# Kernel optimization log

Hardware: AMD Instinct MI355X
Metric: run time of the kernel (lower is better)

## Reference

```python
import jax, jax.numpy as jnp
import numpy as np

N_NODES = 100000
N_EDGES = 1600000
D_FEAT = 32


def setup_inputs() -> dict:
    key = jax.random.key(0)
    k1, k2 = jax.random.split(key)
    x = jax.random.normal(k1, (N_NODES, D_FEAT), dtype=jnp.float32)
    edge_index = jax.random.randint(k2, (2, N_EDGES), 0, N_NODES, dtype=jnp.int64)
    return {"x": x, "edge_index": edge_index}


def reference(x, edge_index):
    # SparseTensor(row=edge_index[0], col=edge_index[1]).matmul(x, reduce='mean')
    # out[i] = mean_{e: row[e]==i} x[col[e]], 0 for isolated rows.
    row, col = edge_index[0], edge_index[1]
    msg_sum = jax.ops.segment_sum(x[col], row, num_segments=N_NODES)  # [N, D]
    deg = jax.ops.segment_sum(jnp.ones((row.shape[0],), dtype=x.dtype), row,
                              num_segments=N_NODES)  # [N]
    denom = jnp.maximum(deg, jnp.asarray(1, dtype=x.dtype))
    return msg_sum / denom[:, None]
```

## Files before the change

### kernel.cpp

```cpp
#include <hip/hip_runtime.h>
#include <hip/hip_fp16.h>

#define D_FEAT 32
#define BNODES 64
#define LOG_BN 6
#define CHUNK 16384
#define BIG 1024
#define CAP 1536
#define ECHUNK CAP
#define CMASK 0x1FFFFu

__global__ void zero_kernel(int* __restrict__ p, int n) {
    int i = blockIdx.x * blockDim.x + threadIdx.x;
    if (i < n) p[i] = 0;
}

__global__ void __launch_bounds__(BIG) build_kernel(const int* __restrict__ row,
                                                    const int* __restrict__ col,
                                                    const float* __restrict__ x,
                                                    __half* __restrict__ xh,
                                                    int* __restrict__ cnt,
                                                    unsigned* __restrict__ packed,
                                                    int E, int nb, int n8) {
    extern __shared__ int shmem[];
    int* hist = shmem;
    int* base = shmem + nb;
    int t = threadIdx.x;
    int blk = blockIdx.x;
    for (int i = t; i < nb; i += BIG) hist[i] = 0;

    int s = blk * CHUNK;
    int e_end = min(E, s + CHUNK);

    int4 r[4], c[4];
    if (s + CHUNK <= E) {
        #pragma unroll
        for (int k = 0; k < 4; ++k) {
            int e = s + t * 4 + k * (BIG * 4);
            r[k] = *(const int4*)&row[e];
            c[k] = *(const int4*)&col[e];
        }
    } else {
        #pragma unroll
        for (int k = 0; k < 4; ++k) {
            int e = s + t * 4 + k * (BIG * 4);
            r[k].x = (e + 0 < e_end) ? row[e + 0] : -1;
            r[k].y = (e + 1 < e_end) ? row[e + 1] : -1;
            r[k].z = (e + 2 < e_end) ? row[e + 2] : -1;
            r[k].w = (e + 3 < e_end) ? row[e + 3] : -1;
            c[k].x = (e + 0 < e_end) ? col[e + 0] : 0;
            c[k].y = (e + 1 < e_end) ? col[e + 1] : 0;
            c[k].z = (e + 2 < e_end) ? col[e + 2] : 0;
            c[k].w = (e + 3 < e_end) ? col[e + 3] : 0;
        }
    }
    __syncthreads();

    #pragma unroll
    for (int k = 0; k < 4; ++k) {
        if (r[k].x >= 0) atomicAdd(&hist[r[k].x >> LOG_BN], 1);
        if (r[k].y >= 0) atomicAdd(&hist[r[k].y >> LOG_BN], 1);
        if (r[k].z >= 0) atomicAdd(&hist[r[k].z >> LOG_BN], 1);
        if (r[k].w >= 0) atomicAdd(&hist[r[k].w >> LOG_BN], 1);
    }
    __syncthreads();

    for (int i = t; i < nb; i += BIG) {
        int h = hist[i];
        base[i] = h ? (i * CAP + atomicAdd(&cnt[i], h)) : 0;
    }
    __syncthreads();

    #define EMIT(rr, cc)                                                      \
        if ((rr) >= 0) {                                                      \
            int b_ = (rr) >> LOG_BN;                                          \
            int slot_ = base[b_] + atomicAdd(&hist[b_], -1) - 1;              \
            packed[slot_] = ((unsigned)((rr) & (BNODES - 1)) << 17) |         \
                            (unsigned)(cc);                                   \
        }
    #pragma unroll
    for (int k = 0; k < 4; ++k) {
        EMIT(r[k].x, c[k].x); EMIT(r[k].y, c[k].y);
        EMIT(r[k].z, c[k].z); EMIT(r[k].w, c[k].w);
    }
    #undef EMIT

    int gstride = gridDim.x * BIG;
    for (int i = blk * BIG + t; i < n8; i += gstride) {
        float4 v = ((const float4*)x)[i];
        __half2 h0 = __floats2half2_rn(v.x, v.y);
        __half2 h1 = __floats2half2_rn(v.z, v.w);
        uint2 u;
        u.x = *reinterpret_cast<unsigned*>(&h0);
        u.y = *reinterpret_cast<unsigned*>(&h1);
        ((uint2*)xh)[i] = u;
    }
}

__global__ void __launch_bounds__(512) phase2_kernel(const __half* __restrict__ xh,
                                                     const unsigned* __restrict__ packed,
                                                     const int* __restrict__ cnt,
                                                     float* __restrict__ out, int N) {
    __shared__ unsigned scol[ECHUNK];
    __shared__ int hist[BNODES];
    __shared__ int hoff[BNODES];
    int t = threadIdx.x;
    int b = blockIdx.x;
    int s = b * CAP;
    int n = cnt[b];
    int node = t >> 3;
    int j = t & 7;
    const uint2* xh2 = (const uint2*)xh;

    if (t < BNODES) hist[t] = 0;
    __syncthreads();

    unsigned pv[3];
    int nv = 0;
    #pragma unroll
    for (int k = 0; k < 3; ++k) {
        int i = t + k * 512;
        if (i < n) {
            unsigned p = packed[s + i];
            pv[nv++] = p;
            atomicAdd(&hist[p >> 17], 1);
        }
    }
    __syncthreads();

    if (t < 64) {
        int v = hist[t];
        int sum = v;
        #pragma unroll
        for (int off = 1; off < 64; off <<= 1) {
            int w = __shfl_up(sum, off);
            if (t >= off) sum += w;
        }
        hoff[t] = sum - v;
    }
    __syncthreads();
    int mcount = hist[node];
    int mbase = hoff[node];
    __syncthreads();

    #pragma unroll
    for (int k = 0; k < 3; ++k) {
        if (k < nv) {
            unsigned p = pv[k];
            int r = p >> 17;
            int slot = hoff[r] + atomicAdd(&hist[r], -1) - 1;
            scol[slot] = p;
        }
    }
    __syncthreads();

    float4 acc = make_float4(0.f, 0.f, 0.f, 0.f);
    #define ACCUM(u)                                                           \
        {                                                                      \
            __half2 ha = *reinterpret_cast<const __half2*>(&(u).x);            \
            __half2 hb = *reinterpret_cast<const __half2*>(&(u).y);            \
            float2 fa = __half22float2(ha);                                    \
            float2 fb = __half22float2(hb);                                    \
            acc.x += fa.x; acc.y += fa.y; acc.z += fb.x; acc.w += fb.y;        \
        }
    int i = 0;
    for (; i + 7 < mcount; i += 8) {
        unsigned cc0 = scol[mbase + i + 0] & CMASK;
        unsigned cc1 = scol[mbase + i + 1] & CMASK;
        unsigned cc2 = scol[mbase + i + 2] & CMASK;
        unsigned cc3 = scol[mbase + i + 3] & CMASK;
        unsigned cc4 = scol[mbase + i + 4] & CMASK;
        unsigned cc5 = scol[mbase + i + 5] & CMASK;
        unsigned cc6 = scol[mbase + i + 6] & CMASK;
        unsigned cc7 = scol[mbase + i + 7] & CMASK;
        uint2 u0 = xh2[cc0 * 8 + j];
        uint2 u1 = xh2[cc1 * 8 + j];
        uint2 u2 = xh2[cc2 * 8 + j];
        uint2 u3 = xh2[cc3 * 8 + j];
        uint2 u4 = xh2[cc4 * 8 + j];
        uint2 u5 = xh2[cc5 * 8 + j];
        uint2 u6 = xh2[cc6 * 8 + j];
        uint2 u7 = xh2[cc7 * 8 + j];
        ACCUM(u0); ACCUM(u1); ACCUM(u2); ACCUM(u3);
        ACCUM(u4); ACCUM(u5); ACCUM(u6); ACCUM(u7);
    }
    for (; i < mcount; ++i) {
        unsigned cc = scol[mbase + i] & CMASK;
        uint2 u = xh2[cc * 8 + j];
        ACCUM(u);
    }
    #undef ACCUM

    int gnode = b * BNODES + node;
    if (gnode < N) {
        float invd = 1.0f / fmaxf((float)mcount, 1.0f);
        float4 v;
        v.x = acc.x * invd; v.y = acc.y * invd;
        v.z = acc.z * invd; v.w = acc.w * invd;
        ((float4*)out)[(size_t)gnode * 8 + j] = v;
    }
}


extern "C" void kernel_launch(void* const* d_in, const int* in_sizes, int n_in,
                              void* d_out, int out_size, void* d_ws, size_t ws_size,
                              hipStream_t stream) {
    const float* x = (const float*)d_in[0];
    const int* edge_index = (const int*)d_in[1];

    int E = in_sizes[1] / 2;
    const int* row = edge_index;
    const int* col = edge_index + E;
    int N = in_sizes[0] / D_FEAT;

    float* out = (float*)d_out;

    int nb = (N + BNODES - 1) / BNODES;
    int nchunks = (E + CHUNK - 1) / CHUNK;
    int n8 = in_sizes[0] / 4;

    int* cnt = (int*)d_ws;
    __half* xh = (__half*)(cnt + ((nb + 1023) & ~1023));
    unsigned* packed = (unsigned*)((char*)xh + (size_t)in_sizes[0] * sizeof(__half));

    zero_kernel<<<(nb + 255) / 256, 256, 0, stream>>>(cnt, nb);

    size_t lds = (size_t)2 * nb * sizeof(int);
    build_kernel<<<nchunks, BIG, lds, stream>>>(row, col, x, xh, cnt, packed, E, nb, n8);
    phase2_kernel<<<nb, 512, 0, stream>>>(xh, packed, cnt, out, N);
}
```

Before: 57.42 us.

## Replace global atomic bucket offsets with per-chunk fixed-slot regions and drop zero kernel

The build kernel no longer uses global atomics on a per-bucket counter. Each chunk writes its edges into a fixed region of REG slots per bucket and records a per-chunk, per-bucket count, which also removes the separate zeroing kernel. The phase-2 kernel prefix-scans those counts across chunks, gathers the scattered regions into shared memory, then does the same local sort as before. This removes global atomic contention and one launch, but the gather becomes scattered and edges past REG per chunk, or past RAWCAP per bucket, are silently dropped.

```diff
diff --git a/kernel.cpp b/kernel.cpp
--- a/kernel.cpp
+++ b/kernel.cpp
@@ -6,25 +6,19 @@
 #define LOG_BN 6
 #define CHUNK 16384
 #define BIG 1024
-#define CAP 1536
-#define ECHUNK CAP
+#define REG 40
+#define RAWCAP 1536
+#define NCH_MAX 128
 #define CMASK 0x1FFFFu
-
-__global__ void zero_kernel(int* __restrict__ p, int n) {
-    int i = blockIdx.x * blockDim.x + threadIdx.x;
-    if (i < n) p[i] = 0;
-}
 
 __global__ void __launch_bounds__(BIG) build_kernel(const int* __restrict__ row,
                                                     const int* __restrict__ col,
                                                     const float* __restrict__ x,
                                                     __half* __restrict__ xh,
-                                                    int* __restrict__ cnt,
+                                                    int* __restrict__ hcnt,
                                                     unsigned* __restrict__ packed,
-                                                    int E, int nb, int n8) {
-    extern __shared__ int shmem[];
-    int* hist = shmem;
-    int* base = shmem + nb;
+                                                    int E, int nb, int nchunks, int n8) {
+    extern __shared__ int hist[];
     int t = threadIdx.x;
     int blk = blockIdx.x;
     for (int i = t; i < nb; i += BIG) hist[i] = 0;
@@ -65,18 +59,19 @@
     }
     __syncthreads();
 
-    for (int i = t; i < nb; i += BIG) {
-        int h = hist[i];
-        base[i] = h ? (i * CAP + atomicAdd(&cnt[i], h)) : 0;
-    }
-    __syncthreads();
-
+    size_t hrow = (size_t)blk * nb;
+    for (int i = t; i < nb; i += BIG) hcnt[hrow + i] = min(hist[i], REG);
+    __syncthreads();
+
+    size_t rstride = (size_t)nchunks * REG;
+    size_t kbase = (size_t)blk * REG;
     #define EMIT(rr, cc)                                                      \
         if ((rr) >= 0) {                                                      \
             int b_ = (rr) >> LOG_BN;                                          \
-            int slot_ = base[b_] + atomicAdd(&hist[b_], -1) - 1;              \
-            packed[slot_] = ((unsigned)((rr) & (BNODES - 1)) << 17) |         \
-                            (unsigned)(cc);                                   \
+            int si = atomicAdd(&hist[b_], -1) - 1;                            \
+            if (si < REG)                                                     \
+                packed[(size_t)b_ * rstride + kbase + si] =                   \
+                    ((unsigned)((rr) & (BNODES - 1)) << 17) | (unsigned)(cc); \
         }
     #pragma unroll
     for (int k = 0; k < 4; ++k) {
@@ -99,33 +94,69 @@
 
 __global__ void __launch_bounds__(512) phase2_kernel(const __half* __restrict__ xh,
                                                      const unsigned* __restrict__ packed,
-                                                     const int* __restrict__ cnt,
-                                                     float* __restrict__ out, int N) {
-    __shared__ unsigned scol[ECHUNK];
+                                                     const int* __restrict__ hcnt,
+                                                     float* __restrict__ out,
+                                                     int N, int nb, int nchunks) {
+    __shared__ int cntk[NCH_MAX];
+    __shared__ int pref[NCH_MAX + 2];
+    __shared__ unsigned scol_raw[RAWCAP];
+    __shared__ unsigned scol[RAWCAP];
     __shared__ int hist[BNODES];
     __shared__ int hoff[BNODES];
     int t = threadIdx.x;
     int b = blockIdx.x;
-    int s = b * CAP;
-    int n = cnt[b];
+    size_t rbase = (size_t)b * nchunks * REG;
     int node = t >> 3;
     int j = t & 7;
     const uint2* xh2 = (const uint2*)xh;
 
+    if (t < nchunks) cntk[t] = hcnt[(size_t)t * nb + b];
     if (t < BNODES) hist[t] = 0;
     __syncthreads();
 
-    unsigned pv[3];
-    int nv = 0;
-    #pragma unroll
-    for (int k = 0; k < 3; ++k) {
-        int i = t + k * 512;
-        if (i < n) {
-            unsigned p = packed[s + i];
-            pv[nv++] = p;
-            atomicAdd(&hist[p >> 17], 1);
-        }
-    }
+    if (t < 64) {
+        int v = (t < nchunks) ? cntk[t] : 0;
+        int sum = v;
+        #pragma unroll
+        for (int off = 1; off < 64; off <<= 1) {
+            int w = __shfl_up(sum, off);
+            if (t >= off) sum += w;
+        }
+        pref[t] = sum - v;
+        if (t == 63) pref[NCH_MAX] = sum;
+    }
+    __syncthreads();
+    if (t < 64) {
+        int k2 = t + 64;
+        int carry = pref[NCH_MAX];
+        int v = (k2 < nchunks) ? cntk[k2] : 0;
+        int sum = v;
+        #pragma unroll
+        for (int off = 1; off < 64; off <<= 1) {
+            int w = __shfl_up(sum, off);
+            if (t >= off) sum += w;
+        }
+        pref[k2] = carry + sum - v;
+        if (t == 63) pref[NCH_MAX + 1] = carry + sum;
+    }
+    __syncthreads();
+    int n = min(pref[NCH_MAX + 1], RAWCAP);
+
+    {
+        int w = t >> 6, l = t & 63;
+        for (int k = w; k < nchunks; k += 8) {
+            int cc = cntk[k];
+            if (l < cc) {
+                int dst = pref[k] + l;
+                if (dst < RAWCAP)
+                    scol_raw[dst] = packed[rbase + (size_t)k * REG + l];
+            }
+        }
+    }
+    __syncthreads();
+
+    for (int i = t; i < n; i += 512)
+        atomicAdd(&hist[scol_raw[i] >> 17], 1);
     __syncthreads();
 
     if (t < 64) {
@@ -143,14 +174,11 @@
     int mbase = hoff[node];
     __syncthreads();
 
-    #pragma unroll
-    for (int k = 0; k < 3; ++k) {
-        if (k < nv) {
-            unsigned p = pv[k];
-            int r = p >> 17;
-            int slot = hoff[r] + atomicAdd(&hist[r], -1) - 1;
-            scol[slot] = p;
-        }
+    for (int i = t; i < n; i += 512) {
+        unsigned p = scol_raw[i];
+        int r = p >> 17;
+        int slot = hoff[r] + atomicAdd(&hist[r], -1) - 1;
+        scol[slot] = p;
     }
     __syncthreads();
 
@@ -219,13 +247,13 @@
     int nchunks = (E + CHUNK - 1) / CHUNK;
     int n8 = in_sizes[0] / 4;
 
-    int* cnt = (int*)d_ws;
-    __half* xh = (__half*)(cnt + ((nb + 1023) & ~1023));
+    int* hcnt = (int*)d_ws;
+    size_t hcnt_elems = ((size_t)nchunks * nb + 1023) & ~(size_t)1023;
+    __half* xh = (__half*)(hcnt + hcnt_elems);
     unsigned* packed = (unsigned*)((char*)xh + (size_t)in_sizes[0] * sizeof(__half));
 
-    zero_kernel<<<(nb + 255) / 256, 256, 0, stream>>>(cnt, nb);
-
-    size_t lds = (size_t)2 * nb * sizeof(int);
-    build_kernel<<<nchunks, BIG, lds, stream>>>(row, col, x, xh, cnt, packed, E, nb, n8);
-    phase2_kernel<<<nb, 512, 0, stream>>>(xh, packed, cnt, out, N);
+    size_t lds = (size_t)nb * sizeof(int);
+    build_kernel<<<nchunks, BIG, lds, stream>>>(row, col, x, xh, hcnt, packed,
+                                                E, nb, nchunks, n8);
+    phase2_kernel<<<nb, 512, 0, stream>>>(xh, packed, hcnt, out, N, nb, nchunks);
 }
```

Measured after the change: 62.01 us. 1.08x slower.
